# Kernel tuning notes

Hardware: AMD Instinct MI355X
Metric: run time of the kernel (lower is better)

Reference implementation:

```python
import jax, jax.numpy as jnp
import numpy as np

N_NODES = 50000
N_EDGES = 800000
IN_CH = 128
OUT_CH = 64
HID_CH = 2 * OUT_CH  # 128


def gcn_conv(x, edge_index, W, b, n_nodes):
    """PyG GCNConv: linear -> add self-loops -> sym-normalized scatter-add -> bias."""
    h = x @ W  # [N, out]
    loop = jnp.arange(n_nodes)
    row = jnp.concatenate([edge_index[0], loop])  # source nodes
    col = jnp.concatenate([edge_index[1], loop])  # target nodes
    deg = jax.ops.segment_sum(jnp.ones_like(col, dtype=h.dtype), col, num_segments=n_nodes)
    dinv = jnp.where(deg > 0, jax.lax.rsqrt(jnp.maximum(deg, 1.0)), 0.0)
    norm = dinv[row] * dinv[col]  # [E+N]
    msg = h[row] * norm[:, None]  # gather + scale, [E+N, out]
    out = jax.ops.segment_sum(msg, col, num_segments=n_nodes)  # scatter-add
    return out + b


def setup_inputs() -> dict:
    key = jax.random.key(0)
    ks = jax.random.split(key, 9)
    x = jax.random.normal(ks[0], (N_NODES, IN_CH), dtype=jnp.float32)
    edge_index = jax.random.randint(ks[1], (2, N_EDGES), 0, N_NODES, dtype=jnp.int64)
    s_in = 1.0 / np.sqrt(IN_CH)
    s_hid = 1.0 / np.sqrt(HID_CH)
    W1 = jax.random.normal(ks[2], (IN_CH, HID_CH), dtype=jnp.float32) * s_in
    b1 = jnp.zeros((HID_CH,), dtype=jnp.float32)
    W2 = jax.random.normal(ks[3], (HID_CH, OUT_CH), dtype=jnp.float32) * s_hid
    b2 = jnp.zeros((OUT_CH,), dtype=jnp.float32)
    W3 = jax.random.normal(ks[4], (HID_CH, OUT_CH), dtype=jnp.float32) * s_hid
    b3 = jnp.zeros((OUT_CH,), dtype=jnp.float32)
    return {"x": x, "edge_index": edge_index, "W1": W1, "b1": b1,
            "W2": W2, "b2": b2, "W3": W3, "b3": b3}


def reference(x, edge_index, W1, b1, W2, b2, W3, b3):
    act = jax.nn.relu
    hidden = act(gcn_conv(x, edge_index, W1, b1, N_NODES))
    x1 = act(gcn_conv(hidden, edge_index, W2, b2, N_NODES))
    x2 = act(gcn_conv(hidden, edge_index, W3, b3, N_NODES))
    return (x1, x2)
```

## Files before the change

kernel.cpp:

```cpp
#include <hip/hip_runtime.h>

#define N_NODES 50000
#define N_EDGES 800000
#define CH 128
#define WT_PAD 136
#define DUMMY N_NODES
#define SLOT_LOG 6
#define AGG_HALF_BLKS 1563

typedef __attribute__((ext_vector_type(8))) short short8;
typedef __attribute__((ext_vector_type(4))) float floatx4;

__device__ __forceinline__ short f2bf(float f) {
    union { float f; unsigned u; } v; v.f = f;
    unsigned r = v.u + 0x7fff + ((v.u >> 16) & 1);
    return (short)(r >> 16);
}
__device__ __forceinline__ float bflo(unsigned u) {
    union { unsigned u; float f; } v; v.u = u << 16; return v.f;
}
__device__ __forceinline__ float bfhi(unsigned u) {
    union { unsigned u; float f; } v; v.u = u & 0xffff0000u; return v.f;
}


__global__ __launch_bounds__(256) void prep_kernel(const float* __restrict__ W1,
                                                   const float* __restrict__ W2,
                                                   const float* __restrict__ W3,
                                                   const float* __restrict__ b2,
                                                   const float* __restrict__ b3,
                                                   unsigned short* __restrict__ Wt1,
                                                   unsigned short* __restrict__ Wt23,
                                                   float* __restrict__ b23,
                                                   int* __restrict__ counts,
                                                   float* __restrict__ dinv,
                                                   unsigned int* __restrict__ gdummy) {
    int i = blockIdx.x * blockDim.x + threadIdx.x;
    if (i < 128 * 128) {
        int n = i >> 7, k = i & 127;
        Wt1[i] = (unsigned short)f2bf(W1[k * 128 + n]);
        float w = (n < 64) ? W2[k * 64 + n] : W3[k * 64 + (n - 64)];
        Wt23[i] = (unsigned short)f2bf(w);
    } else if (i < 128 * 128 + 128) {
        int k2 = i - 128 * 128;
        b23[k2] = (k2 < 64) ? b2[k2] : b3[k2 - 64];
    } else if (i < 128 * 128 + 192) {
        gdummy[i - (128 * 128 + 128)] = 0;
    }
    for (int j = i; j < N_NODES; j += 66 * 256) {
        counts[j] = 0;
        dinv[j] = 1.0f;
    }
}


__global__ void rank_kernel(const int* __restrict__ ei, int* __restrict__ counts,
                            unsigned* __restrict__ rankdst) {
    int e = blockIdx.x * blockDim.x + threadIdx.x;
    if (e < N_EDGES) {
        int dst = ei[N_EDGES + e];
        int r = atomicAdd(&counts[dst], 1);
        rankdst[e] = ((unsigned)r << 16) | (unsigned)dst;
    }
}

__global__ void scatter_plain(const int* __restrict__ ei, const int* __restrict__ counts,
                              const unsigned* __restrict__ rankdst,
                              unsigned short* __restrict__ sorted_src,
                              float* __restrict__ dinv) {
    int e = blockIdx.x * blockDim.x + threadIdx.x;
    if (e < N_EDGES) {
        int src = ei[e];
        unsigned p = rankdst[e];
        int dst = (int)(p & 0xffffu);
        int r = (int)(p >> 16);
        int deg = counts[dst];
        int base = dst << SLOT_LOG;
        if (r < 64) sorted_src[base + r] = (unsigned short)src;
        if (r == 0) dinv[dst] = rsqrtf((float)(deg + 1));
        if (r == deg - 1) {
            int pc = (deg + 3) & ~3;
            if (pc > 64) pc = 64;
            for (int q = deg; q < pc; ++q) sorted_src[base + q] = (unsigned short)DUMMY;
        }
    }
}


template <bool A_BF16>
__global__ __launch_bounds__(256) void gemm_mfma(const void* __restrict__ Ain,
                                                 const unsigned short* __restrict__ Wt,
                                                 const float* __restrict__ dinv,
                                                 unsigned short* __restrict__ g) {
    __shared__ unsigned short lds[128 * WT_PAD];
    int tid = threadIdx.x;
    int wave = tid >> 6, lane = tid & 63;
    int quad = lane >> 4, ln = lane & 15;

    {
        int r = tid >> 1, h = tid & 1;
        const int4* src = (const int4*)(Wt + r * 128 + h * 64);
#pragma unroll
        for (int i = 0; i < 8; ++i)
            *(int4*)&lds[r * WT_PAD + h * 64 + i * 8] = src[i];
    }

    int row_base = blockIdx.x * 64 + wave * 16;
    int arow = row_base + ln;
    bool ok = arow < N_NODES;
    short8 afrag[4];
    if (A_BF16) {
        const unsigned short* A = (const unsigned short*)Ain;
#pragma unroll
        for (int kk = 0; kk < 4; ++kk) {
            short8 v = {};
            if (ok) v = *(const short8*)(A + arow * 128 + kk * 32 + quad * 8);
            afrag[kk] = v;
        }
    } else {
        const float* A = (const float*)Ain;
#pragma unroll
        for (int kk = 0; kk < 4; ++kk) {
            short8 v = {};
            if (ok) {
                const float* p = A + arow * 128 + kk * 32 + quad * 8;
#pragma unroll
                for (int j = 0; j < 8; ++j) v[j] = f2bf(p[j]);
            }
            afrag[kk] = v;
        }
    }
    __syncthreads();

    floatx4 acc[8] = {};
#pragma unroll
    for (int n0 = 0; n0 < 8; ++n0) {
#pragma unroll
        for (int kk = 0; kk < 4; ++kk) {
            short8 b = *(const short8*)&lds[(n0 * 16 + ln) * WT_PAD + kk * 32 + quad * 8];
            acc[n0] = __builtin_amdgcn_mfma_f32_16x16x32_bf16(afrag[kk], b, acc[n0], 0, 0, 0);
        }
    }

    __syncthreads();
    unsigned short* st = &lds[wave * 16 * WT_PAD];
    float dv[4];
#pragma unroll
    for (int r = 0; r < 4; ++r) {
        int node = row_base + quad * 4 + r;
        dv[r] = (node < N_NODES) ? dinv[node] : 0.f;
    }
#pragma unroll
    for (int n0 = 0; n0 < 8; ++n0)
#pragma unroll
        for (int r = 0; r < 4; ++r)
            st[(quad * 4 + r) * WT_PAD + n0 * 16 + ln] =
                (unsigned short)f2bf(acc[n0][r] * dv[r]);
    __syncthreads();

#pragma unroll
    for (int i = 0; i < 4; ++i) {
        int row = i * 4 + quad;
        int node = row_base + row;
        short8 v = *(const short8*)&st[row * WT_PAD + ln * 8];
        if (node < N_NODES) *(short8*)(g + node * 128 + ln * 8) = v;
    }
}


template <int MODE>
__global__ __launch_bounds__(256) void aggregate_bf16(const unsigned short* __restrict__ g,
                                                      const float* __restrict__ dinv,
                                                      const int* __restrict__ degs,
                                                      const unsigned short* __restrict__ srcs,
                                                      const float* __restrict__ bias,
                                                      void* __restrict__ outp) {
    int h = 0, nb = blockIdx.x;
    if (nb >= AGG_HALF_BLKS) { h = 1; nb -= AGG_HALF_BLKS; }
    int n = nb * 32 + (threadIdx.x >> 3);
    if (n >= N_NODES) return;
    int c4 = threadIdx.x & 7;
    int hoff = h * 8;
    const uint4* grow = (const uint4*)g;
    uint4 u = grow[n * 16 + hoff + c4];
    float a0 = bflo(u.x), a1 = bfhi(u.x), a2 = bflo(u.y), a3 = bfhi(u.y);
    float a4 = bflo(u.z), a5 = bfhi(u.z), a6 = bflo(u.w), a7 = bfhi(u.w);
    float c0 = 0.f, c1 = 0.f, c2 = 0.f, c3 = 0.f, c5 = 0.f, c6 = 0.f, c7 = 0.f, c8 = 0.f;
    int beg = n << SLOT_LOG;
    int pend = beg + ((degs[n] + 3) & ~3);
    int e = beg;
    for (; e + 8 <= pend; e += 8) {
        ushort4 sa = *(const ushort4*)&srcs[e];
        ushort4 sb = *(const ushort4*)&srcs[e + 4];
        uint4 v0 = grow[sa.x * 16 + hoff + c4];
        uint4 v1 = grow[sa.y * 16 + hoff + c4];
        uint4 v2 = grow[sa.z * 16 + hoff + c4];
        uint4 v3 = grow[sa.w * 16 + hoff + c4];
        uint4 v4 = grow[sb.x * 16 + hoff + c4];
        uint4 v5 = grow[sb.y * 16 + hoff + c4];
        uint4 v6 = grow[sb.z * 16 + hoff + c4];
        uint4 v7 = grow[sb.w * 16 + hoff + c4];
        a0 += bflo(v0.x); a1 += bfhi(v0.x); a2 += bflo(v0.y); a3 += bfhi(v0.y);
        a4 += bflo(v0.z); a5 += bfhi(v0.z); a6 += bflo(v0.w); a7 += bfhi(v0.w);
        c0 += bflo(v1.x); c1 += bfhi(v1.x); c2 += bflo(v1.y); c3 += bfhi(v1.y);
        c5 += bflo(v1.z); c6 += bfhi(v1.z); c7 += bflo(v1.w); c8 += bfhi(v1.w);
        a0 += bflo(v2.x); a1 += bfhi(v2.x); a2 += bflo(v2.y); a3 += bfhi(v2.y);
        a4 += bflo(v2.z); a5 += bfhi(v2.z); a6 += bflo(v2.w); a7 += bfhi(v2.w);
        c0 += bflo(v3.x); c1 += bfhi(v3.x); c2 += bflo(v3.y); c3 += bfhi(v3.y);
        c5 += bflo(v3.z); c6 += bfhi(v3.z); c7 += bflo(v3.w); c8 += bfhi(v3.w);
        a0 += bflo(v4.x); a1 += bfhi(v4.x); a2 += bflo(v4.y); a3 += bfhi(v4.y);
        a4 += bflo(v4.z); a5 += bfhi(v4.z); a6 += bflo(v4.w); a7 += bfhi(v4.w);
        c0 += bflo(v5.x); c1 += bfhi(v5.x); c2 += bflo(v5.y); c3 += bfhi(v5.y);
        c5 += bflo(v5.z); c6 += bfhi(v5.z); c7 += bflo(v5.w); c8 += bfhi(v5.w);
        a0 += bflo(v6.x); a1 += bfhi(v6.x); a2 += bflo(v6.y); a3 += bfhi(v6.y);
        a4 += bflo(v6.z); a5 += bfhi(v6.z); a6 += bflo(v6.w); a7 += bfhi(v6.w);
        c0 += bflo(v7.x); c1 += bfhi(v7.x); c2 += bflo(v7.y); c3 += bfhi(v7.y);
        c5 += bflo(v7.z); c6 += bfhi(v7.z); c7 += bflo(v7.w); c8 += bfhi(v7.w);
    }
    if (e < pend) {
        ushort4 sa = *(const ushort4*)&srcs[e];
        uint4 v0 = grow[sa.x * 16 + hoff + c4];
        uint4 v1 = grow[sa.y * 16 + hoff + c4];
        uint4 v2 = grow[sa.z * 16 + hoff + c4];
        uint4 v3 = grow[sa.w * 16 + hoff + c4];
        a0 += bflo(v0.x); a1 += bfhi(v0.x); a2 += bflo(v0.y); a3 += bfhi(v0.y);
        a4 += bflo(v0.z); a5 += bfhi(v0.z); a6 += bflo(v0.w); a7 += bfhi(v0.w);
        c0 += bflo(v1.x); c1 += bfhi(v1.x); c2 += bflo(v1.y); c3 += bfhi(v1.y);
        c5 += bflo(v1.z); c6 += bfhi(v1.z); c7 += bflo(v1.w); c8 += bfhi(v1.w);
        a0 += bflo(v2.x); a1 += bfhi(v2.x); a2 += bflo(v2.y); a3 += bfhi(v2.y);
        a4 += bflo(v2.z); a5 += bfhi(v2.z); a6 += bflo(v2.w); a7 += bfhi(v2.w);
        c0 += bflo(v3.x); c1 += bfhi(v3.x); c2 += bflo(v3.y); c3 += bfhi(v3.y);
        c5 += bflo(v3.z); c6 += bfhi(v3.z); c7 += bflo(v3.w); c8 += bfhi(v3.w);
    }
    a0 += c0; a1 += c1; a2 += c2; a3 += c3; a4 += c5; a5 += c6; a6 += c7; a7 += c8;
    float d = dinv[n];
    float4 bv0 = ((const float4*)bias)[h * 16 + c4 * 2];
    float4 bv1 = ((const float4*)bias)[h * 16 + c4 * 2 + 1];
    float o0 = fmaxf(d * a0 + bv0.x, 0.f);
    float o1 = fmaxf(d * a1 + bv0.y, 0.f);
    float o2 = fmaxf(d * a2 + bv0.z, 0.f);
    float o3 = fmaxf(d * a3 + bv0.w, 0.f);
    float o4 = fmaxf(d * a4 + bv1.x, 0.f);
    float o5 = fmaxf(d * a5 + bv1.y, 0.f);
    float o6 = fmaxf(d * a6 + bv1.z, 0.f);
    float o7 = fmaxf(d * a7 + bv1.w, 0.f);
    if (MODE == 0) {
        uint4 w;
        w.x = ((unsigned)(unsigned short)f2bf(o0)) | (((unsigned)(unsigned short)f2bf(o1)) << 16);
        w.y = ((unsigned)(unsigned short)f2bf(o2)) | (((unsigned)(unsigned short)f2bf(o3)) << 16);
        w.z = ((unsigned)(unsigned short)f2bf(o4)) | (((unsigned)(unsigned short)f2bf(o5)) << 16);
        w.w = ((unsigned)(unsigned short)f2bf(o6)) | (((unsigned)(unsigned short)f2bf(o7)) << 16);
        ((uint4*)outp)[n * 16 + hoff + c4] = w;
    } else {
        float* out = (float*)outp + (size_t)h * N_NODES * 64;
        ((float4*)out)[n * 16 + c4 * 2] = make_float4(o0, o1, o2, o3);
        ((float4*)out)[n * 16 + c4 * 2 + 1] = make_float4(o4, o5, o6, o7);
    }
}


extern "C" void kernel_launch(void* const* d_in, const int* in_sizes, int n_in,
                              void* d_out, int out_size, void* d_ws, size_t ws_size,
                              hipStream_t stream) {
    const float* x  = (const float*)d_in[0];
    const int*   ei = (const int*)d_in[1];
    const float* W1 = (const float*)d_in[2];
    const float* b1 = (const float*)d_in[3];
    const float* W2 = (const float*)d_in[4];
    const float* b2 = (const float*)d_in[5];
    const float* W3 = (const float*)d_in[6];
    const float* b3 = (const float*)d_in[7];
    float* out = (float*)d_out;

    char* w = (char*)d_ws;
    int*            counts     = (int*)(w + 0);
    float*          dinv       = (float*)(w + 204800);
    unsigned*       rankdst    = (unsigned*)(w + 409600);
    unsigned short* sorted_src = (unsigned short*)(w + 3686400);
    unsigned short* Wt1        = (unsigned short*)(w + 10485760);
    unsigned short* Wt23       = (unsigned short*)(w + 10518528);
    float*          b23        = (float*)(w + 10551296);
    unsigned short* g1         = (unsigned short*)(w + 12582912);
    unsigned short* hidden     = (unsigned short*)(w + 25690112);

    prep_kernel<<<66, 256, 0, stream>>>(W1, W2, W3, b2, b3, Wt1, Wt23, b23, counts, dinv,
                                        (unsigned int*)(g1 + N_NODES * 128));
    rank_kernel<<<(N_EDGES + 255) / 256, 256, 0, stream>>>(ei, counts, rankdst);
    scatter_plain<<<(N_EDGES + 255) / 256, 256, 0, stream>>>(ei, counts, rankdst,
                                                             sorted_src, dinv);

    const int gemm_blocks = (N_NODES + 63) / 64;
    const int agg_blocks = 2 * AGG_HALF_BLKS;

    gemm_mfma<false><<<gemm_blocks, 256, 0, stream>>>(x, Wt1, dinv, g1);
    aggregate_bf16<0><<<agg_blocks, 256, 0, stream>>>(g1, dinv, counts, sorted_src, b1, hidden);

    gemm_mfma<true><<<gemm_blocks, 256, 0, stream>>>(hidden, Wt23, dinv, g1);
    aggregate_bf16<1><<<agg_blocks, 256, 0, stream>>>(g1, dinv, counts, sorted_src, b23, out);
}
```

Baseline: 213.9 us.

## Fuse rank and scatter into one atomic pass, recompute dinv from degrees

Replaces the two-pass edge bucketing (rank then scatter) with a single kernel that writes each source straight into its slot from the atomic rank. The slot array is pre-filled with the dummy index in the prep kernel, so no pad loop is needed. The dinv array is dropped, and rsqrt(deg+1) is recomputed in the GEMM and aggregate kernels. It also adds vectorized float4 loads in the fp32 GEMM path and nontemporal loads and stores. In exchange, prep must now fill the whole 6.4 MB slot array, which adds write traffic.

```diff
diff --git a/kernel.cpp b/kernel.cpp
--- a/kernel.cpp
+++ b/kernel.cpp
@@ -7,6 +7,7 @@
 #define DUMMY N_NODES
 #define SLOT_LOG 6
 #define AGG_HALF_BLKS 1563
+#define PREP_THREADS (128 * 256)
 
 typedef __attribute__((ext_vector_type(8))) short short8;
 typedef __attribute__((ext_vector_type(4))) float floatx4;
@@ -33,7 +34,7 @@
                                                    unsigned short* __restrict__ Wt23,
                                                    float* __restrict__ b23,
                                                    int* __restrict__ counts,
-                                                   float* __restrict__ dinv,
+                                                   unsigned short* __restrict__ sorted_src,
                                                    unsigned int* __restrict__ gdummy) {
     int i = blockIdx.x * blockDim.x + threadIdx.x;
     if (i < 128 * 128) {
@@ -47,42 +48,22 @@
     } else if (i < 128 * 128 + 192) {
         gdummy[i - (128 * 128 + 128)] = 0;
     }
-    for (int j = i; j < N_NODES; j += 66 * 256) {
-        counts[j] = 0;
-        dinv[j] = 1.0f;
-    }
-}
-
-
-__global__ void rank_kernel(const int* __restrict__ ei, int* __restrict__ counts,
-                            unsigned* __restrict__ rankdst) {
+    for (int j = i; j < N_NODES; j += PREP_THREADS) counts[j] = 0;
+    const unsigned dpat = ((unsigned)DUMMY) | (((unsigned)DUMMY) << 16);
+    uint4 dfill = make_uint4(dpat, dpat, dpat, dpat);
+    uint4* sp = (uint4*)sorted_src;
+    for (int j = i; j < (N_NODES << SLOT_LOG) / 8; j += PREP_THREADS) sp[j] = dfill;
+}
+
+
+__global__ void rank_scatter(const int* __restrict__ ei, int* __restrict__ counts,
+                             unsigned short* __restrict__ sorted_src) {
     int e = blockIdx.x * blockDim.x + threadIdx.x;
     if (e < N_EDGES) {
-        int dst = ei[N_EDGES + e];
+        int src = __builtin_nontemporal_load(ei + e);
+        int dst = __builtin_nontemporal_load(ei + N_EDGES + e);
         int r = atomicAdd(&counts[dst], 1);
-        rankdst[e] = ((unsigned)r << 16) | (unsigned)dst;
-    }
-}
-
-__global__ void scatter_plain(const int* __restrict__ ei, const int* __restrict__ counts,
-                              const unsigned* __restrict__ rankdst,
-                              unsigned short* __restrict__ sorted_src,
-                              float* __restrict__ dinv) {
-    int e = blockIdx.x * blockDim.x + threadIdx.x;
-    if (e < N_EDGES) {
-        int src = ei[e];
-        unsigned p = rankdst[e];
-        int dst = (int)(p & 0xffffu);
-        int r = (int)(p >> 16);
-        int deg = counts[dst];
-        int base = dst << SLOT_LOG;
-        if (r < 64) sorted_src[base + r] = (unsigned short)src;
-        if (r == 0) dinv[dst] = rsqrtf((float)(deg + 1));
-        if (r == deg - 1) {
-            int pc = (deg + 3) & ~3;
-            if (pc > 64) pc = 64;
-            for (int q = deg; q < pc; ++q) sorted_src[base + q] = (unsigned short)DUMMY;
-        }
+        if (r < 64) sorted_src[(dst << SLOT_LOG) + r] = (unsigned short)src;
     }
 }
 
@@ -90,7 +71,7 @@
 template <bool A_BF16>
 __global__ __launch_bounds__(256) void gemm_mfma(const void* __restrict__ Ain,
                                                  const unsigned short* __restrict__ Wt,
-                                                 const float* __restrict__ dinv,
+                                                 const int* __restrict__ degs,
                                                  unsigned short* __restrict__ g) {
     __shared__ unsigned short lds[128 * WT_PAD];
     int tid = threadIdx.x;
@@ -123,9 +104,10 @@
         for (int kk = 0; kk < 4; ++kk) {
             short8 v = {};
             if (ok) {
-                const float* p = A + arow * 128 + kk * 32 + quad * 8;
-#pragma unroll
-                for (int j = 0; j < 8; ++j) v[j] = f2bf(p[j]);
+                const floatx4* p = (const floatx4*)(A + arow * 128 + kk * 32 + quad * 8);
+                floatx4 fa = p[0], fb = p[1];
+                v[0] = f2bf(fa.x); v[1] = f2bf(fa.y); v[2] = f2bf(fa.z); v[3] = f2bf(fa.w);
+                v[4] = f2bf(fb.x); v[5] = f2bf(fb.y); v[6] = f2bf(fb.z); v[7] = f2bf(fb.w);
             }
             afrag[kk] = v;
         }
@@ -148,7 +130,7 @@
 #pragma unroll
     for (int r = 0; r < 4; ++r) {
         int node = row_base + quad * 4 + r;
-        dv[r] = (node < N_NODES) ? dinv[node] : 0.f;
+        dv[r] = (node < N_NODES) ? rsqrtf((float)(degs[node] + 1)) : 0.f;
     }
 #pragma unroll
     for (int n0 = 0; n0 < 8; ++n0)
@@ -170,7 +152,6 @@
 
 template <int MODE>
 __global__ __launch_bounds__(256) void aggregate_bf16(const unsigned short* __restrict__ g,
-                                                      const float* __restrict__ dinv,
                                                       const int* __restrict__ degs,
                                                       const unsigned short* __restrict__ srcs,
                                                       const float* __restrict__ bias,
@@ -186,8 +167,9 @@
     float a0 = bflo(u.x), a1 = bfhi(u.x), a2 = bflo(u.y), a3 = bfhi(u.y);
     float a4 = bflo(u.z), a5 = bfhi(u.z), a6 = bflo(u.w), a7 = bfhi(u.w);
     float c0 = 0.f, c1 = 0.f, c2 = 0.f, c3 = 0.f, c5 = 0.f, c6 = 0.f, c7 = 0.f, c8 = 0.f;
+    int deg = degs[n];
     int beg = n << SLOT_LOG;
-    int pend = beg + ((degs[n] + 3) & ~3);
+    int pend = beg + ((deg + 3) & ~3);
     int e = beg;
     for (; e + 8 <= pend; e += 8) {
         ushort4 sa = *(const ushort4*)&srcs[e];
@@ -233,7 +215,7 @@
         c5 += bflo(v3.z); c6 += bfhi(v3.z); c7 += bflo(v3.w); c8 += bfhi(v3.w);
     }
     a0 += c0; a1 += c1; a2 += c2; a3 += c3; a4 += c5; a5 += c6; a6 += c7; a7 += c8;
-    float d = dinv[n];
+    float d = rsqrtf((float)(deg + 1));
     float4 bv0 = ((const float4*)bias)[h * 16 + c4 * 2];
     float4 bv1 = ((const float4*)bias)[h * 16 + c4 * 2 + 1];
     float o0 = fmaxf(d * a0 + bv0.x, 0.f);
@@ -253,8 +235,11 @@
         ((uint4*)outp)[n * 16 + hoff + c4] = w;
     } else {
         float* out = (float*)outp + (size_t)h * N_NODES * 64;
-        ((float4*)out)[n * 16 + c4 * 2] = make_float4(o0, o1, o2, o3);
-        ((float4*)out)[n * 16 + c4 * 2 + 1] = make_float4(o4, o5, o6, o7);
+        floatx4* o = (floatx4*)out + n * 16 + c4 * 2;
+        floatx4 w0; w0.x = o0; w0.y = o1; w0.z = o2; w0.w = o3;
+        floatx4 w1; w1.x = o4; w1.y = o5; w1.z = o6; w1.w = o7;
+        __builtin_nontemporal_store(w0, o);
+        __builtin_nontemporal_store(w1, o + 1);
     }
 }
 
@@ -274,8 +259,6 @@
 
     char* w = (char*)d_ws;
     int*            counts     = (int*)(w + 0);
-    float*          dinv       = (float*)(w + 204800);
-    unsigned*       rankdst    = (unsigned*)(w + 409600);
     unsigned short* sorted_src = (unsigned short*)(w + 3686400);
     unsigned short* Wt1        = (unsigned short*)(w + 10485760);
     unsigned short* Wt23       = (unsigned short*)(w + 10518528);
@@ -283,18 +266,16 @@
     unsigned short* g1         = (unsigned short*)(w + 12582912);
     unsigned short* hidden     = (unsigned short*)(w + 25690112);
 
-    prep_kernel<<<66, 256, 0, stream>>>(W1, W2, W3, b2, b3, Wt1, Wt23, b23, counts, dinv,
-                                        (unsigned int*)(g1 + N_NODES * 128));
-    rank_kernel<<<(N_EDGES + 255) / 256, 256, 0, stream>>>(ei, counts, rankdst);
-    scatter_plain<<<(N_EDGES + 255) / 256, 256, 0, stream>>>(ei, counts, rankdst,
-                                                             sorted_src, dinv);
+    prep_kernel<<<128, 256, 0, stream>>>(W1, W2, W3, b2, b3, Wt1, Wt23, b23, counts,
+                                         sorted_src, (unsigned int*)(g1 + N_NODES * 128));
+    rank_scatter<<<(N_EDGES + 255) / 256, 256, 0, stream>>>(ei, counts, sorted_src);
 
     const int gemm_blocks = (N_NODES + 63) / 64;
     const int agg_blocks = 2 * AGG_HALF_BLKS;
 
-    gemm_mfma<false><<<gemm_blocks, 256, 0, stream>>>(x, Wt1, dinv, g1);
-    aggregate_bf16<0><<<agg_blocks, 256, 0, stream>>>(g1, dinv, counts, sorted_src, b1, hidden);
-
-    gemm_mfma<true><<<gemm_blocks, 256, 0, stream>>>(hidden, Wt23, dinv, g1);
-    aggregate_bf16<1><<<agg_blocks, 256, 0, stream>>>(g1, dinv, counts, sorted_src, b23, out);
-}
+    gemm_mfma<false><<<gemm_blocks, 256, 0, stream>>>(x, Wt1, counts, g1);
+    aggregate_bf16<0><<<agg_blocks, 256, 0, stream>>>(g1, counts, sorted_src, b1, hidden);
+
+    gemm_mfma<true><<<gemm_blocks, 256, 0, stream>>>(hidden, Wt23, counts, g1);
+    aggregate_bf16<1><<<agg_blocks, 256, 0, stream>>>(g1, counts, sorted_src, b23, out);
+}
```

Measured after the change: 209.3 us. 1.02x faster.
